# Kernel tuning notes

Measured on AMD Instinct MI355X. Metric: run time of the kernel, lower is better.

The kernel has to match this reference:

```python
import jax, jax.numpy as jnp
import numpy as np

B, S, T = 256, 120, 24   # batch, src frames, predicted frames
D, H = 216, 1024          # input_dim (24 joints x 3x3 rotmat), hidden_dim


def setup_inputs() -> dict:
    key = jax.random.key(0)
    ks = jax.random.split(key, 8)
    s = 0.05  # ~ init_weights uniform(-0.08, 0.08) scale
    return {
        "src": jax.random.normal(ks[0], (B, S, D), jnp.float32),
        "tgt": jax.random.normal(ks[1], (B, T, D), jnp.float32),
        "W_ih": jax.random.normal(ks[2], (4 * H, D), jnp.float32) * s,
        "W_hh": jax.random.normal(ks[3], (4 * H, H), jnp.float32) * s,
        "b_ih": jnp.zeros((4 * H,), jnp.float32),
        "b_hh": jnp.zeros((4 * H,), jnp.float32),
        "W_out": jax.random.normal(ks[4], (D, H), jnp.float32) * s,
        "b_out": jnp.zeros((D,), jnp.float32),
        "max_len": T,
    }


def reference(src, tgt, W_ih, W_hh, b_ih, b_hh, W_out, b_out, max_len):
    # Eval-mode forward: dropout = identity.
    # Encoder: teacher-forced (teacher_forcing_ratio=1.0 -> always feed src[t]).
    def cell(x, h, c):
        # PyTorch LSTM gate order: i, f, g, o
        gates = x @ W_ih.T + b_ih + h @ W_hh.T + b_hh  # [B, 4H]
        i, f, g, o = jnp.split(gates, 4, axis=-1)
        c = jax.nn.sigmoid(f) * c + jax.nn.sigmoid(i) * jnp.tanh(g)
        h = jax.nn.sigmoid(o) * jnp.tanh(c)
        return h, c

    b = src.shape[0]
    h0 = jnp.zeros((b, H), src.dtype)
    c0 = jnp.zeros((b, H), src.dtype)

    # Encoder over src, time-major [S, B, D]
    def enc_step(carry, x):
        h, c = carry
        h, c = cell(x, h, c)
        return (h, c), None

    (h, c), _ = jax.lax.scan(enc_step, (h0, c0), jnp.swapaxes(src, 0, 1))

    # Decoder: first input is last src frame, then feed back projected output
    def dec_step(carry, _):
        h, c, x = carry
        h, c = cell(x, h, c)
        out = h @ W_out.T + b_out  # [B, D]
        return (h, c, out), out

    _, outs = jax.lax.scan(dec_step, (h, c, src[:, -1, :]), None, length=max_len)
    return jnp.swapaxes(outs, 0, 1)  # [B, max_len, D]
```

## Files before the change

kernel.cpp:

```cpp
#include <hip/hip_runtime.h>
#include <hip/hip_bf16.h>

typedef unsigned short u16;
typedef unsigned int   u32;
typedef unsigned long long u64;
typedef __attribute__((ext_vector_type(4)))  float  f32x4;
typedef __attribute__((ext_vector_type(8)))  short  short8;
typedef __attribute__((ext_vector_type(16))) float  f32x16;

#define MB     256
#define SRCT   120
#define DECT   24
#define NSTEP  144
#define DIN    216
#define HDIM   1024
#define KXP    224
#define KA     1248
#define NGATE  4096
#define OUTD   216
#define NWG    256

#define OFF_SRCBF 0u
#define OFF_H     13762560u
#define OFF_XDEC  14811136u
#define OFF_WCAT  14925824u
#define OFF_WO    25149440u
#define OFF_BAR   25591808u

__device__ __forceinline__ u16 f2bf(float f) {
    union { float f; unsigned v; } c; c.f = f;
    return (u16)((c.v + 0x7FFFu + ((c.v >> 16) & 1u)) >> 16);
}
__device__ __forceinline__ float sigm(float x)  { return 1.0f / (1.0f + __expf(-x)); }
__device__ __forceinline__ float tanh_(float x) { return 1.0f - 2.0f / (1.0f + __expf(2.0f * x)); }

__device__ __forceinline__ void pstore(u64* p, u64 v) { *p = v; }

__device__ __forceinline__ short8 ld_l2(const u16* p) {
    short8 r;
    asm volatile("global_load_dwordx4 %0, %1, off sc0" : "=v"(r) : "v"(p));
    return r;
}
template <int N>
__device__ __forceinline__ void vwait() {
    asm volatile("s_waitcnt vmcnt(%0)" :: "n"(N));
    __builtin_amdgcn_sched_barrier(0);
}

__device__ __forceinline__ void g_arrive(u32* slots, int k) {
    __syncthreads();
    if (threadIdx.x == 0) {
        asm volatile("s_waitcnt vmcnt(0)" ::: "memory");
        __hip_atomic_fetch_add(slots + (k & 63), 1u, __ATOMIC_RELAXED, __HIP_MEMORY_SCOPE_AGENT);
    }
}
__device__ __forceinline__ void g_wait(u32* slots, int k) {
    if (threadIdx.x == 0) {
        const u32 tgt = 32u * (u32)((k >> 6) + 1);
        while (__hip_atomic_load(slots + (k & 63), __ATOMIC_RELAXED, __HIP_MEMORY_SCOPE_AGENT) < tgt)
            __builtin_amdgcn_s_sleep(1);
    }
    __syncthreads();
}

__global__ void prep_kernel(const float* __restrict__ src,
                            const float* __restrict__ W_ih,
                            const float* __restrict__ W_hh,
                            const float* __restrict__ W_out,
                            u16* __restrict__ srcbf, u16* __restrict__ H,
                            u16* __restrict__ Xd,    u16* __restrict__ Wcat,
                            u16* __restrict__ Wo,    u32* __restrict__ bar) {
    const int nS  = SRCT * 8 * 28 * 256;
    const int nW  = NGATE * KA;
    const int nWo = OUTD * HDIM;
    const int nH  = MB * HDIM;
    const int nXd = 8 * 28 * 256;
    const int nB  = 8 * 64;
    const int total = nS + nW + nWo + nH + nXd + nB;
    for (int i = blockIdx.x * blockDim.x + threadIdx.x; i < total; i += gridDim.x * blockDim.x) {
        if (i < nS) {
            int r = i & 255, i2 = i >> 8;
            int m = r >> 3, e = r & 7;
            int oct = i2 % 28, q = i2 / 28;
            int gi = q & 7, t = q >> 3;
            int col = oct * 8 + e, b = gi * 32 + m;
            srcbf[i] = (col < DIN) ? f2bf(src[((size_t)b * SRCT + t) * DIN + col]) : (u16)0;
        } else if (i < nS + nW) {
            int j = i - nS;
            int r = j / KA, col = j % KA;
            u16 v = 0;
            if (col < DIN)       v = f2bf(W_ih[(size_t)r * DIN + col]);
            else if (col >= KXP) v = f2bf(W_hh[(size_t)r * HDIM + (col - KXP)]);
            Wcat[j] = v;
        } else if (i < nS + nW + nWo) {
            int j = i - nS - nW;
            Wo[j] = f2bf(W_out[j]);
        } else if (i < nS + nW + nWo + nH) {
            H[i - nS - nW - nWo] = 0;
        } else if (i < nS + nW + nWo + nH + nXd) {
            Xd[i - nS - nW - nWo - nH] = 0;
        } else {
            bar[i - nS - nW - nWo - nH - nXd] = 0;
        }
    }
}

template <int J>
__device__ __forceinline__ void gate_issue(short8 (&av)[20], const u16* xb, const u16* hb,
                                           int ktb, int lo) {
    int kt = ktb + J;
    if (kt > 77) kt = 77;
    const int o2 = 2 * kt;
    const u16* base = (o2 < 28) ? (xb + o2 * 256) : (hb + (o2 - 28) * 256);
    av[J] = ld_l2(base + lo);
}
template <int J>
__device__ __forceinline__ void gate_pro(short8 (&av)[20], const u16* xb, const u16* hb,
                                         int ktb, int lo) {
    gate_issue<J>(av, xb, hb, ktb, lo);
    if constexpr (J + 1 < 8) gate_pro<J + 1>(av, xb, hb, ktb, lo);
}
template <int J>
__device__ __forceinline__ void gate_body(short8 (&av)[20], short8 (&Bf)[4][20], f32x16 (&acc)[4],
                                          const u16* xb, const u16* hb, int ktb, int lo) {
    if constexpr (J + 8 < 20) gate_issue<J + 8>(av, xb, hb, ktb, lo);
    vwait<(J + 8 < 20) ? 8 : (19 - J)>();
    acc[0] = __builtin_amdgcn_mfma_f32_32x32x16_bf16(av[J], Bf[0][J], acc[0], 0, 0, 0);
    acc[1] = __builtin_amdgcn_mfma_f32_32x32x16_bf16(av[J], Bf[1][J], acc[1], 0, 0, 0);
    acc[2] = __builtin_amdgcn_mfma_f32_32x32x16_bf16(av[J], Bf[2][J], acc[2], 0, 0, 0);
    acc[3] = __builtin_amdgcn_mfma_f32_32x32x16_bf16(av[J], Bf[3][J], acc[3], 0, 0, 0);
    if constexpr (J + 1 < 20) gate_body<J + 1>(av, Bf, acc, xb, hb, ktb, lo);
}

template <int J>
__device__ __forceinline__ void out_issue(short8 (&av)[16], const u16* hb, int kt0, int lo) {
    const int o2 = 2 * (kt0 + J);
    av[J] = ld_l2(hb + o2 * 256 + lo);
}
template <int J>
__device__ __forceinline__ void out_pro(short8 (&av)[16], const u16* hb, int kt0, int lo) {
    out_issue<J>(av, hb, kt0, lo);
    if constexpr (J + 1 < 8) out_pro<J + 1>(av, hb, kt0, lo);
}
template <int J>
__device__ __forceinline__ void out_body(short8 (&av)[16], f32x16& oacc, const u16* hb,
                                         const u16* wob, int kt0, int lo) {
    if constexpr (J + 8 < 16) out_issue<J + 8>(av, hb, kt0, lo);
    vwait<(J + 8 < 16) ? 8 : (15 - J)>();
    short8 bf = *(const short8*)(wob + (size_t)(kt0 + J) * 16);
    oacc = __builtin_amdgcn_mfma_f32_32x32x16_bf16(av[J], bf, oacc, 0, 0, 0);
    if constexpr (J + 1 < 16) out_body<J + 1>(av, oacc, hb, wob, kt0, lo);
}

__global__ void __launch_bounds__(256, 1)
lstm_persist(const u16* __restrict__ srcbf, u16* __restrict__ H,
             u16* __restrict__ Xd, const u16* __restrict__ Wcat,
             const u16* __restrict__ Wo,
             const float* __restrict__ b_ih, const float* __restrict__ b_hh,
             const float* __restrict__ b_out,
             float* __restrict__ dout, u32* __restrict__ bar)
{
    __shared__ __align__(16) float G2[16 * 32 * 36];
    __shared__ __align__(16) u16  Hx[4 * 32 * 8];
    __shared__ __align__(16) char lds_pad[8192];
    __shared__ int gs_share[2];

    const int tid  = threadIdx.x;
    const int p    = tid >> 6;
    const int lane = tid & 63;
    const int l31  = lane & 31;
    const int kg   = lane >> 5;
    const int lo   = kg * 256 + l31 * 8;

    if (tid == 255) *(volatile char*)lds_pad = 0;

    if (tid == 0) {
        u32 xcc;
        asm volatile("s_getreg_b32 %0, hwreg(HW_REG_XCC_ID)" : "=s"(xcc));
        u32 myidx = __hip_atomic_fetch_add((u32*)Xd + xcc, 1u,
                                           __ATOMIC_RELAXED, __HIP_MEMORY_SCOPE_AGENT);
        gs_share[0] = (int)xcc;
        gs_share[1] = (int)myidx;
    }
    __syncthreads();
    const int g  = gs_share[0];
    const int s  = gs_share[1];
    const int b0 = g * 32;

    u32* gslots = bar + g * 64;
    u16* Xdg = Xd + (size_t)g * 7168;

    const int ktb = p * 20 - (p == 3 ? 1 : 0);
    const int ktc = (p < 2) ? 20 : 19;

    short8 Bfrag[4][20];
#pragma unroll
    for (int gg = 0; gg < 4; ++gg) {
        const u16* pw = Wcat + (size_t)(gg * 1024 + s * 32 + l31) * KA + kg * 8;
#pragma unroll
        for (int j = 0; j < 20; ++j) {
            if (j < ktc) {
                int kt = ktb + j;
                Bfrag[gg][j] = *(const short8*)(pw + (size_t)kt * 16);
            } else {
                Bfrag[gg][j] = short8{};
            }
        }
    }

    const int cs = tid & 31;
    const int bq = tid >> 5;
    float creg[4] = {0.f, 0.f, 0.f, 0.f};
    const int hcg = s * 32 + cs;
    const float bI  = b_ih[hcg]        + b_hh[hcg];
    const float bF  = b_ih[1024 + hcg] + b_hh[1024 + hcg];
    const float bG_ = b_ih[2048 + hcg] + b_hh[2048 + hcg];
    const float bO  = b_ih[3072 + hcg] + b_hh[3072 + hcg];
    const float bOutv = (s < 7 && hcg < OUTD) ? b_out[hcg] : 0.f;

    for (int t = 0; t < NSTEP; ++t) {
        const u16* hb    = H + (size_t)(t & 1) * (MB * HDIM) + (size_t)g * 32768;
        u16*       HTn   = H + (size_t)((t + 1) & 1) * (MB * HDIM);
        const u16* hnext = HTn + (size_t)g * 32768;
        const u16* xb;
        if (t < SRCT)       xb = srcbf + (size_t)(t * 8 + g) * 7168;
        else if (t == SRCT) xb = srcbf + (size_t)((SRCT - 1) * 8 + g) * 7168;
        else                xb = Xdg;

        f32x16 acc[4] = {f32x16{}, f32x16{}, f32x16{}, f32x16{}};
        {
            short8 av[20];
            gate_pro<0>(av, xb, hb, ktb, lo);
            gate_body<0>(av, Bfrag, acc, xb, hb, ktb, lo);
        }
#pragma unroll
        for (int gg = 0; gg < 4; ++gg) {
#pragma unroll
            for (int rq = 0; rq < 4; ++rq) {
                f32x4 v;
                v[0] = acc[gg][rq * 4 + 0]; v[1] = acc[gg][rq * 4 + 1];
                v[2] = acc[gg][rq * 4 + 2]; v[3] = acc[gg][rq * 4 + 3];
                *(f32x4*)&G2[(size_t)((gg * 4 + p) * 32 + l31) * 36 + rq * 8 + kg * 4] = v;
            }
        }
        __syncthreads();

        {
            f32x4 sg[4];
#pragma unroll
            for (int gg = 0; gg < 4; ++gg) {
                f32x4 a = *(const f32x4*)&G2[(size_t)((gg * 4 + 0) * 32 + cs) * 36 + bq * 4];
#pragma unroll
                for (int pp = 1; pp < 4; ++pp)
                    a += *(const f32x4*)&G2[(size_t)((gg * 4 + pp) * 32 + cs) * 36 + bq * 4];
                sg[gg] = a;
            }
#pragma unroll
            for (int i = 0; i < 4; ++i) {
                float gi = sg[0][i] + bI, gf = sg[1][i] + bF;
                float gG = sg[2][i] + bG_, go = sg[3][i] + bO;
                float c = sigm(gf) * creg[i] + sigm(gi) * tanh_(gG);
                creg[i] = c;
                Hx[(cs >> 3) * 256 + (bq * 4 + i) * 8 + (cs & 7)] = f2bf(sigm(go) * tanh_(c));
            }
        }
        __syncthreads();
        pstore((u64*)HTn + (size_t)g * 8192 + s * 256 + tid, ((const u64*)Hx)[tid]);

        if (t < SRCT) {
            g_arrive(gslots, t);
            g_wait(gslots, t);
        } else {
            const int d  = t - SRCT;
            const int k1 = SRCT + 2 * d;
            g_arrive(gslots, k1);
            g_wait(gslots, k1);
            if (s < 7) {
                f32x16 oacc = {};
                const int orow = (s * 32 + l31 < OUTD) ? (s * 32 + l31) : (OUTD - 1);
                const u16* wob = Wo + (size_t)orow * HDIM + kg * 8;
                short8 av2[16];
                out_pro<0>(av2, hnext, p * 16, lo);
                out_body<0>(av2, oacc, hnext, wob, p * 16, lo);
#pragma unroll
                for (int rq = 0; rq < 4; ++rq) {
                    f32x4 v;
                    v[0] = oacc[rq * 4 + 0]; v[1] = oacc[rq * 4 + 1];
                    v[2] = oacc[rq * 4 + 2]; v[3] = oacc[rq * 4 + 3];
                    *(f32x4*)&G2[(size_t)(p * 32 + l31) * 36 + rq * 8 + kg * 4] = v;
                }
            }
            __syncthreads();
            if (s < 7) {
                const int  ocol = s * 32 + cs;
                const bool real = ocol < OUTD;
                f32x4 S = *(const f32x4*)&G2[(size_t)(0 * 32 + cs) * 36 + bq * 4];
#pragma unroll
                for (int pp = 1; pp < 4; ++pp)
                    S += *(const f32x4*)&G2[(size_t)(pp * 32 + cs) * 36 + bq * 4];
#pragma unroll
                for (int i = 0; i < 4; ++i) {
                    float v = real ? (S[i] + bOutv) : 0.f;
                    Hx[(cs >> 3) * 256 + (bq * 4 + i) * 8 + (cs & 7)] = real ? f2bf(v) : (u16)0;
                    if (real)
                        dout[(size_t)(b0 + bq * 4 + i) * (DECT * OUTD) + (size_t)d * OUTD + ocol] = v;
                }
            }
            __syncthreads();
            if (s < 7)
                pstore((u64*)Xdg + s * 256 + tid, ((const u64*)Hx)[tid]);
            if (t < NSTEP - 1) {
                g_arrive(gslots, k1 + 1);
                g_wait(gslots, k1 + 1);
            }
        }
    }
}

extern "C" void kernel_launch(void* const* d_in, const int* in_sizes, int n_in,
                              void* d_out, int out_size, void* d_ws, size_t ws_size,
                              hipStream_t stream) {
    const float* src   = (const float*)d_in[0];
    const float* W_ih  = (const float*)d_in[2];
    const float* W_hh  = (const float*)d_in[3];
    const float* b_ih  = (const float*)d_in[4];
    const float* b_hh  = (const float*)d_in[5];
    const float* W_out = (const float*)d_in[6];
    const float* b_out = (const float*)d_in[7];
    float* out = (float*)d_out;

    char* ws = (char*)d_ws;
    u16* srcbf = (u16*)(ws + OFF_SRCBF);
    u16* H     = (u16*)(ws + OFF_H);
    u16* Xd    = (u16*)(ws + OFF_XDEC);
    u16* Wcat  = (u16*)(ws + OFF_WCAT);
    u16* Wo    = (u16*)(ws + OFF_WO);
    u32* bar   = (u32*)(ws + OFF_BAR);

    hipLaunchKernelGGL(prep_kernel, dim3(2048), dim3(256), 0, stream,
                       src, W_ih, W_hh, W_out, srcbf, H, Xd, Wcat, Wo, bar);

    hipLaunchKernelGGL(lstm_persist, dim3(NWG), dim3(256), 0, stream,
                       srcbf, H, Xd, Wcat, Wo, b_ih, b_hh, b_out, out, bar);
}
```

Measured before the change: 860.3 us.

## Split grid barrier into per-wave polled flags and overlap decoder sync with gate loads

Replaces the single-counter group barrier with counters striped over four slots, polled by lanes of every wave instead of thread 0 followed by __syncthreads. The gate GEMM is reordered to load the hidden-state K-range first and the x-input last. The decoder's wait for the projected output is moved into the middle of the gate pipeline, so h@W_hh work proceeds before the new x is ready. Workgroups that do no output projection skip the second wait and just signal. This shortens the serial barrier chain per timestep, at the cost of more polling traffic and subtler ordering correctness.

```diff
diff --git a/kernel.cpp b/kernel.cpp
--- a/kernel.cpp
+++ b/kernel.cpp
@@ -47,20 +47,26 @@
     __builtin_amdgcn_sched_barrier(0);
 }
 
-__device__ __forceinline__ void g_arrive(u32* slots, int k) {
+__device__ __forceinline__ void flag_add(u32* slots, int k, int s) {
+    __hip_atomic_fetch_add(slots + (s & 3) * 32 + (k & 7), 1u,
+                           __ATOMIC_RELAXED, __HIP_MEMORY_SCOPE_AGENT);
+}
+__device__ __forceinline__ void g_arrive(u32* gslots, int k, int s) {
     __syncthreads();
     if (threadIdx.x == 0) {
         asm volatile("s_waitcnt vmcnt(0)" ::: "memory");
-        __hip_atomic_fetch_add(slots + (k & 63), 1u, __ATOMIC_RELAXED, __HIP_MEMORY_SCOPE_AGENT);
-    }
-}
-__device__ __forceinline__ void g_wait(u32* slots, int k) {
-    if (threadIdx.x == 0) {
-        const u32 tgt = 32u * (u32)((k >> 6) + 1);
-        while (__hip_atomic_load(slots + (k & 63), __ATOMIC_RELAXED, __HIP_MEMORY_SCOPE_AGENT) < tgt)
+        flag_add(gslots, k, s);
+    }
+}
+__device__ __forceinline__ void wave_poll(const u32* gslots, int k) {
+    const u32 tgt = 8u * (u32)((k >> 3) + 1);
+    const int l = threadIdx.x & 63;
+    if (l < 4) {
+        const u32* a = gslots + l * 32 + (k & 7);
+        while (__hip_atomic_load(a, __ATOMIC_RELAXED, __HIP_MEMORY_SCOPE_AGENT) < tgt)
             __builtin_amdgcn_s_sleep(1);
     }
-    __syncthreads();
+    __builtin_amdgcn_sched_barrier(0);
 }
 
 __global__ void prep_kernel(const float* __restrict__ src,
@@ -75,7 +81,7 @@
     const int nWo = OUTD * HDIM;
     const int nH  = MB * HDIM;
     const int nXd = 8 * 28 * 256;
-    const int nB  = 8 * 64;
+    const int nB  = 8 * 128;
     const int total = nS + nW + nWo + nH + nXd + nB;
     for (int i = blockIdx.x * blockDim.x + threadIdx.x; i < total; i += gridDim.x * blockDim.x) {
         if (i < nS) {
@@ -106,30 +112,37 @@
 }
 
 template <int J>
-__device__ __forceinline__ void gate_issue(short8 (&av)[20], const u16* xb, const u16* hb,
-                                           int ktb, int lo) {
-    int kt = ktb + J;
-    if (kt > 77) kt = 77;
-    const int o2 = 2 * kt;
-    const u16* base = (o2 < 28) ? (xb + o2 * 256) : (hb + (o2 - 28) * 256);
-    av[J] = ld_l2(base + lo);
-}
-template <int J>
-__device__ __forceinline__ void gate_pro(short8 (&av)[20], const u16* xb, const u16* hb,
-                                         int ktb, int lo) {
-    gate_issue<J>(av, xb, hb, ktb, lo);
-    if constexpr (J + 1 < 8) gate_pro<J + 1>(av, xb, hb, ktb, lo);
-}
-template <int J>
-__device__ __forceinline__ void gate_body(short8 (&av)[20], short8 (&Bf)[4][20], f32x16 (&acc)[4],
-                                          const u16* xb, const u16* hb, int ktb, int lo) {
-    if constexpr (J + 8 < 20) gate_issue<J + 8>(av, xb, hb, ktb, lo);
+__device__ __forceinline__ void gate_issue2(short8 (&av)[20], const u16* hbw,
+                                            const u16* xbw, int xcnt) {
+    if constexpr (J < 16) {
+        av[J] = ld_l2(hbw + J * 512);
+    } else {
+        int xt = J - 16; if (xt >= xcnt) xt = xcnt - 1;
+        av[J] = ld_l2(xbw + xt * 512);
+    }
+}
+template <int J>
+__device__ __forceinline__ void gate_pro2(short8 (&av)[20], const u16* hbw,
+                                          const u16* xbw, int xcnt) {
+    gate_issue2<J>(av, hbw, xbw, xcnt);
+    if constexpr (J + 1 < 8) gate_pro2<J + 1>(av, hbw, xbw, xcnt);
+}
+template <int J>
+__device__ __forceinline__ void gate_body2(short8 (&av)[20], short8 (&Bf)[4][20], f32x16 (&acc)[4],
+                                           const u16* hbw, const u16* xbw, int xcnt,
+                                           const u32* gslots, int pollk) {
+    if constexpr (J + 8 < 20) {
+        if constexpr (J + 8 == 16) {
+            if (pollk >= 0) wave_poll(gslots, pollk);
+        }
+        gate_issue2<J + 8>(av, hbw, xbw, xcnt);
+    }
     vwait<(J + 8 < 20) ? 8 : (19 - J)>();
     acc[0] = __builtin_amdgcn_mfma_f32_32x32x16_bf16(av[J], Bf[0][J], acc[0], 0, 0, 0);
     acc[1] = __builtin_amdgcn_mfma_f32_32x32x16_bf16(av[J], Bf[1][J], acc[1], 0, 0, 0);
     acc[2] = __builtin_amdgcn_mfma_f32_32x32x16_bf16(av[J], Bf[2][J], acc[2], 0, 0, 0);
     acc[3] = __builtin_amdgcn_mfma_f32_32x32x16_bf16(av[J], Bf[3][J], acc[3], 0, 0, 0);
-    if constexpr (J + 1 < 20) gate_body<J + 1>(av, Bf, acc, xb, hb, ktb, lo);
+    if constexpr (J + 1 < 20) gate_body2<J + 1>(av, Bf, acc, hbw, xbw, xcnt, gslots, pollk);
 }
 
 template <int J>
@@ -187,11 +200,11 @@
     const int s  = gs_share[1];
     const int b0 = g * 32;
 
-    u32* gslots = bar + g * 64;
+    u32* gslots = bar + g * 128;
     u16* Xdg = Xd + (size_t)g * 7168;
 
-    const int ktb = p * 20 - (p == 3 ? 1 : 0);
-    const int ktc = (p < 2) ? 20 : 19;
+    const int xcnt  = (p < 2) ? 4 : 3;
+    const int xbase = p * 4 - (p == 3 ? 1 : 0);
 
     short8 Bfrag[4][20];
 #pragma unroll
@@ -199,12 +212,10 @@
         const u16* pw = Wcat + (size_t)(gg * 1024 + s * 32 + l31) * KA + kg * 8;
 #pragma unroll
         for (int j = 0; j < 20; ++j) {
-            if (j < ktc) {
-                int kt = ktb + j;
-                Bfrag[gg][j] = *(const short8*)(pw + (size_t)kt * 16);
-            } else {
-                Bfrag[gg][j] = short8{};
-            }
+            int kt; bool valid = true;
+            if (j < 16) kt = 14 + p * 16 + j;
+            else { int xt = j - 16; if (xt < xcnt) kt = xbase + xt; else { kt = 0; valid = false; } }
+            Bfrag[gg][j] = valid ? *(const short8*)(pw + (size_t)kt * 16) : short8{};
         }
     }
 
@@ -227,11 +238,17 @@
         else if (t == SRCT) xb = srcbf + (size_t)((SRCT - 1) * 8 + g) * 7168;
         else                xb = Xdg;
 
+        const int upk   = (t > SRCT && s >= 7) ? (2 * t - SRCT - 2) : -1;
+        const int pollk = (t > SRCT)           ? (2 * t - SRCT - 1) : -1;
+        if (upk >= 0) wave_poll(gslots, upk);
+
         f32x16 acc[4] = {f32x16{}, f32x16{}, f32x16{}, f32x16{}};
         {
             short8 av[20];
-            gate_pro<0>(av, xb, hb, ktb, lo);
-            gate_body<0>(av, Bfrag, acc, xb, hb, ktb, lo);
+            const u16* hbw = hb + p * 8192 + lo;
+            const u16* xbw = xb + (size_t)xbase * 512 + lo;
+            gate_pro2<0>(av, hbw, xbw, xcnt);
+            gate_body2<0>(av, Bfrag, acc, hbw, xbw, xcnt, gslots, pollk);
         }
 #pragma unroll
         for (int gg = 0; gg < 4; ++gg) {
@@ -268,14 +285,14 @@
         pstore((u64*)HTn + (size_t)g * 8192 + s * 256 + tid, ((const u64*)Hx)[tid]);
 
         if (t < SRCT) {
-            g_arrive(gslots, t);
-            g_wait(gslots, t);
+            g_arrive(gslots, t, s);
+            wave_poll(gslots, t);
         } else {
             const int d  = t - SRCT;
             const int k1 = SRCT + 2 * d;
-            g_arrive(gslots, k1);
-            g_wait(gslots, k1);
+            g_arrive(gslots, k1, s);
             if (s < 7) {
+                wave_poll(gslots, k1);
                 f32x16 oacc = {};
                 const int orow = (s * 32 + l31 < OUTD) ? (s * 32 + l31) : (OUTD - 1);
                 const u16* wob = Wo + (size_t)orow * HDIM + kg * 8;
@@ -289,29 +306,29 @@
                     v[2] = oacc[rq * 4 + 2]; v[3] = oacc[rq * 4 + 3];
                     *(f32x4*)&G2[(size_t)(p * 32 + l31) * 36 + rq * 8 + kg * 4] = v;
                 }
-            }
-            __syncthreads();
-            if (s < 7) {
-                const int  ocol = s * 32 + cs;
-                const bool real = ocol < OUTD;
-                f32x4 S = *(const f32x4*)&G2[(size_t)(0 * 32 + cs) * 36 + bq * 4];
-#pragma unroll
-                for (int pp = 1; pp < 4; ++pp)
-                    S += *(const f32x4*)&G2[(size_t)(pp * 32 + cs) * 36 + bq * 4];
-#pragma unroll
-                for (int i = 0; i < 4; ++i) {
-                    float v = real ? (S[i] + bOutv) : 0.f;
-                    Hx[(cs >> 3) * 256 + (bq * 4 + i) * 8 + (cs & 7)] = real ? f2bf(v) : (u16)0;
-                    if (real)
-                        dout[(size_t)(b0 + bq * 4 + i) * (DECT * OUTD) + (size_t)d * OUTD + ocol] = v;
+                __syncthreads();
+                {
+                    const int  ocol = s * 32 + cs;
+                    const bool real = ocol < OUTD;
+                    f32x4 S = *(const f32x4*)&G2[(size_t)(0 * 32 + cs) * 36 + bq * 4];
+#pragma unroll
+                    for (int pp = 1; pp < 4; ++pp)
+                        S += *(const f32x4*)&G2[(size_t)(pp * 32 + cs) * 36 + bq * 4];
+#pragma unroll
+                    for (int i = 0; i < 4; ++i) {
+                        float v = real ? (S[i] + bOutv) : 0.f;
+                        Hx[(cs >> 3) * 256 + (bq * 4 + i) * 8 + (cs & 7)] = real ? f2bf(v) : (u16)0;
+                        if (real)
+                            dout[(size_t)(b0 + bq * 4 + i) * (DECT * OUTD) + (size_t)d * OUTD + ocol] = v;
+                    }
                 }
-            }
-            __syncthreads();
-            if (s < 7)
+                __syncthreads();
                 pstore((u64*)Xdg + s * 256 + tid, ((const u64*)Hx)[tid]);
-            if (t < NSTEP - 1) {
-                g_arrive(gslots, k1 + 1);
-                g_wait(gslots, k1 + 1);
+                if (t < NSTEP - 1)
+                    g_arrive(gslots, k1 + 1, s);
+            } else {
+                if (t < NSTEP - 1 && tid == 0)
+                    flag_add(gslots, k1 + 1, s);
             }
         }
     }
```

Result: slower. 1.196 ms (+39.0%).
